# Optimization experiments

Measured on AMD Instinct MI355X. Metric: run time of the kernel, lower is better.

## Reference

```python
import jax, jax.numpy as jnp
import numpy as np

CD_W = 0.2  # chamfer_weight
EPS = 1e-7


def setup_inputs() -> dict:
    key = jax.random.key(0)
    k1, k2, k3, k4, k5 = jax.random.split(key, 5)
    B, N, K = 16, 4096, 4096
    num_add, obj_num_p = 8, 512
    return {
        "adv_pc": jax.random.normal(k1, (B, N, 3), dtype=jnp.float32),
        "ori_pc": jax.random.normal(k2, (B, K, 3), dtype=jnp.float32),
        "adv_obj": jax.random.normal(k3, (B, num_add, obj_num_p, 3), dtype=jnp.float32),
        "ori_obj": jax.random.normal(k4, (B, num_add, obj_num_p, 3), dtype=jnp.float32),
        "weights": jax.random.uniform(k5, (B,), dtype=jnp.float32),
    }


def reference(adv_pc, ori_pc, adv_obj, ori_obj, weights):
    B = adv_pc.shape[0]
    # --- Chamfer (method='adv2ori'): mean over adv points of min squared dist to ori ---
    a2 = jnp.sum(adv_pc * adv_pc, axis=-1)            # [B, N]
    o2 = jnp.sum(ori_pc * ori_pc, axis=-1)            # [B, K]
    cross = jnp.einsum('bnd,bkd->bnk', adv_pc, ori_pc)  # [B, N, K]
    sqdist = a2[:, :, None] + o2[:, None, :] - 2.0 * cross  # [B, N, K]
    loss1 = jnp.mean(jnp.min(sqdist, axis=2), axis=1)  # [B] adv->ori NN sq dist
    chamfer_loss = jnp.mean(loss1 * weights)
    # --- Global L2 dist between flattened adv/ori objects ---
    diff = adv_obj.reshape(B, -1, 3) - ori_obj.reshape(B, -1, 3)
    l2 = jnp.sqrt(jnp.sum(diff * diff, axis=(1, 2)) + EPS)  # [B]
    l2_loss = jnp.mean(l2 * weights)
    return l2_loss + CD_W * chamfer_loss
```

## Files before the change

kernel.cpp:

```cpp
#include <hip/hip_runtime.h>
#include <math.h>

typedef short bf16x8 __attribute__((ext_vector_type(8)));
typedef float f32x16 __attribute__((ext_vector_type(16)));
typedef unsigned int u32x4 __attribute__((ext_vector_type(4)));

#define B 16
#define N 4096
#define K 4096
#define OBJ_ELEMS (8*512*3)
#define OBJ_VEC4  (OBJ_ELEMS/4)
#define NSEG 32
#define NCHUNK (N/NSEG)
#define BLK 512
#define OBJ_V4_PER_BLK (OBJ_VEC4/NSEG)
#define CD_W 0.2f
#define EPS_F 1e-7f

#define CS_OFF 0
#define LS_OFF (B*NSEG)

__device__ __forceinline__ unsigned int cvt_pk_bf16(float lo, float hi) {
    unsigned int r;
    asm volatile("v_cvt_pk_bf16_f32 %0, %1, %2" : "=v"(r) : "v"(lo), "v"(hi));
    return r;
}

__global__ __launch_bounds__(BLK, 4) void chamfer_mfma_kernel(
    const float* __restrict__ adv, const float* __restrict__ ori,
    const float* __restrict__ adv_obj, const float* __restrict__ ori_obj,
    float* __restrict__ csum, float* __restrict__ lsq)
{
    __shared__ uint2 slds[K];
    __shared__ float rowmin[8][32];
    __shared__ float a2lds[NCHUNK];
    __shared__ float red_c[2], red_l[2];

    const int nseg = blockIdx.x;
    const int b    = blockIdx.y;
    const int tid  = threadIdx.x;
    const int wid  = tid >> 6;
    const int lane = tid & 63;
    const int col  = lane & 31;
    const int hi   = lane >> 5;
    const int rg   = wid & 3;
    const int kh   = wid >> 2;

    {
        const float4* src =
            reinterpret_cast<const float4*>(ori + (size_t)(b*K + tid*8)*3);
        float4 f0 = src[0], f1 = src[1], f2 = src[2];
        float4 f3 = src[3], f4 = src[4], f5 = src[5];
        float xs[8], ys[8], zs[8];
        xs[0]=f0.x; ys[0]=f0.y; zs[0]=f0.z;
        xs[1]=f0.w; ys[1]=f1.x; zs[1]=f1.y;
        xs[2]=f1.z; ys[2]=f1.w; zs[2]=f2.x;
        xs[3]=f2.y; ys[3]=f2.z; zs[3]=f2.w;
        xs[4]=f3.x; ys[4]=f3.y; zs[4]=f3.z;
        xs[5]=f3.w; ys[5]=f4.x; zs[5]=f4.y;
        xs[6]=f4.z; ys[6]=f4.w; zs[6]=f5.x;
        xs[7]=f5.y; ys[7]=f5.z; zs[7]=f5.w;
        #pragma unroll
        for (int j = 0; j < 8; ++j) {
            float x = xs[j], y = ys[j], z = zs[j];
            float o2 = x*x + y*y + z*z;
            uint2 e;
            e.x = cvt_pk_bf16(-2.f*x, -2.f*y);
            e.y = cvt_pk_bf16(-2.f*z, o2);
            slds[tid*8 + j] = e;
        }
    }

    const int n = nseg*NCHUNK + rg*32 + col;
    const float* ap = adv + (b*N + n)*3;
    float ax = ap[0], ay = ap[1], az = ap[2];
    float a2 = ax*ax + ay*ay + az*az;
    if (kh == 0 && hi == 0) a2lds[rg*32 + col] = a2;
    unsigned int a01 = 0u, a23 = 0u;
    if (hi == 0) {
        a01 = cvt_pk_bf16(ax, ay);
        a23 = cvt_pk_bf16(az, 1.0f);
    }
    u32x4 aw = {a01, a23, 0u, 0u};
    bf16x8 afrag = __builtin_bit_cast(bf16x8, aw);

    __syncthreads();

    f32x16 acc = {INFINITY,INFINITY,INFINITY,INFINITY,
                  INFINITY,INFINITY,INFINITY,INFINITY,
                  INFINITY,INFINITY,INFINITY,INFINITY,
                  INFINITY,INFINITY,INFINITY,INFINITY};
    const f32x16 zc = {0,0,0,0, 0,0,0,0, 0,0,0,0, 0,0,0,0};
    const float4* s4 = reinterpret_cast<const float4*>(slds);

    #pragma unroll
    for (int ph = 0; ph < 4; ++ph) {
        float4 f[8];
        #pragma unroll
        for (int j = 0; j < 8; ++j)
            f[j] = s4[(kh*32 + ph*8 + j)*32 + col];
        #pragma unroll
        for (int j = 0; j < 8; ++j) {
            u32x4 uu = __builtin_bit_cast(u32x4, f[j]);
            u32x4 w0 = {uu.x, uu.y, 0u, 0u};
            u32x4 w1 = {uu.z, uu.w, 0u, 0u};
            bf16x8 b0 = __builtin_bit_cast(bf16x8, w0);
            bf16x8 b1 = __builtin_bit_cast(bf16x8, w1);
            f32x16 c0 = __builtin_amdgcn_mfma_f32_32x32x16_bf16(afrag, b0, zc, 0,0,0);
            f32x16 c1 = __builtin_amdgcn_mfma_f32_32x32x16_bf16(afrag, b1, zc, 0,0,0);
            #pragma unroll
            for (int r = 0; r < 16; ++r)
                acc[r] = fminf(fminf(c0[r], c1[r]), acc[r]);
        }
    }

    #pragma unroll
    for (int r = 0; r < 16; ++r) {
        float v = acc[r];
        v = fminf(v, __shfl_xor(v, 1));
        v = fminf(v, __shfl_xor(v, 2));
        v = fminf(v, __shfl_xor(v, 4));
        v = fminf(v, __shfl_xor(v, 8));
        v = fminf(v, __shfl_xor(v, 16));
        acc[r] = v;
    }
    if (col == 0) {
        #pragma unroll
        for (int r = 0; r < 16; ++r)
            rowmin[wid][(r&3) + 8*(r>>2) + 4*hi] = acc[r];
    }
    __syncthreads();

    float s = 0.f;
    if (wid < 2) {
        int row = tid;
        int rg2 = row >> 5, ri = row & 31;
        float m = fminf(rowmin[rg2][ri], rowmin[4 + rg2][ri]);
        s = m + a2lds[row];
    } else if (wid < 4) {
        int li = (wid - 2)*64 + lane;
        if (li < OBJ_V4_PER_BLK) {
            int idx = b*OBJ_VEC4 + nseg*OBJ_V4_PER_BLK + li;
            float4 a = reinterpret_cast<const float4*>(adv_obj)[idx];
            float4 o = reinterpret_cast<const float4*>(ori_obj)[idx];
            float dx = a.x - o.x, dy = a.y - o.y, dz = a.z - o.z, dw = a.w - o.w;
            s = dx*dx + dy*dy + dz*dz + dw*dw;
        }
    }
    #pragma unroll
    for (int off = 32; off; off >>= 1) s += __shfl_down(s, off);
    if (lane == 0) {
        if (wid < 2)       red_c[wid]     = s;
        else if (wid < 4)  red_l[wid - 2] = s;
    }
    __syncthreads();
    if (tid == 0) csum[b*NSEG + nseg] = red_c[0] + red_c[1];
    if (tid == 1) lsq [b*NSEG + nseg] = red_l[0] + red_l[1];
}

__global__ __launch_bounds__(256) void final_kernel(
    const float* __restrict__ csum, const float* __restrict__ lsq,
    const float* __restrict__ w, float* __restrict__ out)
{
    const int tid = threadIdx.x;
    float c = csum[2*tid] + csum[2*tid + 1];
    float l = lsq [2*tid] + lsq [2*tid + 1];
    #pragma unroll
    for (int off = 8; off; off >>= 1) {
        c += __shfl_down(c, off, 16);
        l += __shfl_down(l, off, 16);
    }
    __shared__ float sc[B], sl[B];
    int bb = tid >> 4;
    if ((tid & 15) == 0) { sc[bb] = c; sl[bb] = l; }
    __syncthreads();
    if (tid < 64) {
        float cc = 0.f, ll = 0.f;
        if (tid < B) {
            float wt = w[tid];
            cc = (sc[tid] / (float)N) * wt;
            ll = sqrtf(sl[tid] + EPS_F) * wt;
        }
        #pragma unroll
        for (int off = 8; off; off >>= 1) {
            cc += __shfl_down(cc, off);
            ll += __shfl_down(ll, off);
        }
        if (tid == 0) out[0] = ll / (float)B + CD_W * (cc / (float)B);
    }
}

extern "C" void kernel_launch(void* const* d_in, const int* in_sizes, int n_in,
                              void* d_out, int out_size, void* d_ws, size_t ws_size,
                              hipStream_t stream)
{
    const float* adv_pc  = (const float*)d_in[0];
    const float* ori_pc  = (const float*)d_in[1];
    const float* adv_obj = (const float*)d_in[2];
    const float* ori_obj = (const float*)d_in[3];
    const float* weights = (const float*)d_in[4];
    float* out = (float*)d_out;
    float* ws  = (float*)d_ws;

    float* csum = ws + CS_OFF;
    float* lsq  = ws + LS_OFF;

    chamfer_mfma_kernel<<<dim3(NSEG, B), dim3(BLK), 0, stream>>>(
        adv_pc, ori_pc, adv_obj, ori_obj, csum, lsq);

    final_kernel<<<dim3(1), dim3(256), 0, stream>>>(csum, lsq, weights, out);
}
```

Measured before the change: 19.59 us.

## Fuse final reduction into main kernel via atomicAdd, compute L2 in nseg-0 blocks

Drops the separate final reduction kernel. Each block now scales its chamfer partial sum by the weight and constants and atomically adds it to the output, which is zeroed by a memset. The per-batch L2 object norm is computed entirely by the nseg==0 block (six waves, eight float4 loads each) so the sqrt can be applied locally. This trades one kernel launch for a memset, 512 float atomics, and a load imbalance in the nseg==0 blocks.

```diff
diff --git a/kernel.cpp b/kernel.cpp
--- a/kernel.cpp
+++ b/kernel.cpp
@@ -13,12 +13,8 @@
 #define NSEG 32
 #define NCHUNK (N/NSEG)
 #define BLK 512
-#define OBJ_V4_PER_BLK (OBJ_VEC4/NSEG)
 #define CD_W 0.2f
 #define EPS_F 1e-7f
-
-#define CS_OFF 0
-#define LS_OFF (B*NSEG)
 
 __device__ __forceinline__ unsigned int cvt_pk_bf16(float lo, float hi) {
     unsigned int r;
@@ -29,12 +25,12 @@
 __global__ __launch_bounds__(BLK, 4) void chamfer_mfma_kernel(
     const float* __restrict__ adv, const float* __restrict__ ori,
     const float* __restrict__ adv_obj, const float* __restrict__ ori_obj,
-    float* __restrict__ csum, float* __restrict__ lsq)
+    const float* __restrict__ w, float* __restrict__ out)
 {
     __shared__ uint2 slds[K];
     __shared__ float rowmin[8][32];
     __shared__ float a2lds[NCHUNK];
-    __shared__ float red_c[2], red_l[2];
+    __shared__ float red_c[2], red_l[6];
 
     const int nseg = blockIdx.x;
     const int b    = blockIdx.y;
@@ -137,56 +133,34 @@
         int rg2 = row >> 5, ri = row & 31;
         float m = fminf(rowmin[rg2][ri], rowmin[4 + rg2][ri]);
         s = m + a2lds[row];
-    } else if (wid < 4) {
-        int li = (wid - 2)*64 + lane;
-        if (li < OBJ_V4_PER_BLK) {
-            int idx = b*OBJ_VEC4 + nseg*OBJ_V4_PER_BLK + li;
+    } else if (nseg == 0) {
+        int i = (wid - 2)*64 + lane;
+        #pragma unroll
+        for (int j = 0; j < 8; ++j) {
+            int idx = b*OBJ_VEC4 + i + j*384;
             float4 a = reinterpret_cast<const float4*>(adv_obj)[idx];
             float4 o = reinterpret_cast<const float4*>(ori_obj)[idx];
             float dx = a.x - o.x, dy = a.y - o.y, dz = a.z - o.z, dw = a.w - o.w;
-            s = dx*dx + dy*dy + dz*dz + dw*dw;
+            s += dx*dx + dy*dy + dz*dz + dw*dw;
         }
     }
     #pragma unroll
     for (int off = 32; off; off >>= 1) s += __shfl_down(s, off);
     if (lane == 0) {
-        if (wid < 2)       red_c[wid]     = s;
-        else if (wid < 4)  red_l[wid - 2] = s;
+        if (wid < 2) red_c[wid]     = s;
+        else         red_l[wid - 2] = s;
     }
     __syncthreads();
-    if (tid == 0) csum[b*NSEG + nseg] = red_c[0] + red_c[1];
-    if (tid == 1) lsq [b*NSEG + nseg] = red_l[0] + red_l[1];
-}
 
-__global__ __launch_bounds__(256) void final_kernel(
-    const float* __restrict__ csum, const float* __restrict__ lsq,
-    const float* __restrict__ w, float* __restrict__ out)
-{
-    const int tid = threadIdx.x;
-    float c = csum[2*tid] + csum[2*tid + 1];
-    float l = lsq [2*tid] + lsq [2*tid + 1];
-    #pragma unroll
-    for (int off = 8; off; off >>= 1) {
-        c += __shfl_down(c, off, 16);
-        l += __shfl_down(l, off, 16);
-    }
-    __shared__ float sc[B], sl[B];
-    int bb = tid >> 4;
-    if ((tid & 15) == 0) { sc[bb] = c; sl[bb] = l; }
-    __syncthreads();
-    if (tid < 64) {
-        float cc = 0.f, ll = 0.f;
-        if (tid < B) {
-            float wt = w[tid];
-            cc = (sc[tid] / (float)N) * wt;
-            ll = sqrtf(sl[tid] + EPS_F) * wt;
+    if (tid == 0) {
+        float wt = w[b];
+        float contrib = (red_c[0] + red_c[1]) * wt * (CD_W / ((float)B * (float)N));
+        if (nseg == 0) {
+            float lsum = red_l[0] + red_l[1] + red_l[2]
+                       + red_l[3] + red_l[4] + red_l[5];
+            contrib += sqrtf(lsum + EPS_F) * wt / (float)B;
         }
-        #pragma unroll
-        for (int off = 8; off; off >>= 1) {
-            cc += __shfl_down(cc, off);
-            ll += __shfl_down(ll, off);
-        }
-        if (tid == 0) out[0] = ll / (float)B + CD_W * (cc / (float)B);
+        atomicAdd(out, contrib);
     }
 }
 
@@ -200,13 +174,9 @@
     const float* ori_obj = (const float*)d_in[3];
     const float* weights = (const float*)d_in[4];
     float* out = (float*)d_out;
-    float* ws  = (float*)d_ws;
 
-    float* csum = ws + CS_OFF;
-    float* lsq  = ws + LS_OFF;
+    hipMemsetAsync(out, 0, sizeof(float), stream);
 
     chamfer_mfma_kernel<<<dim3(NSEG, B), dim3(BLK), 0, stream>>>(
-        adv_pc, ori_pc, adv_obj, ori_obj, csum, lsq);
-
-    final_kernel<<<dim3(1), dim3(256), 0, stream>>>(csum, lsq, weights, out);
+        adv_pc, ori_pc, adv_obj, ori_obj, weights, out);
 }
```

Result: slower. 24.46 us (+24.8%).

## Prepack ori points to bf16 in separate kernel, read from global instead of LDS

Applied to the files above, without the earlier changes.

Adds a pre-pass kernel that converts ori points into packed bf16 (-2x,-2y,-2z,|o|^2) once per batch and writes them to workspace. The main kernel drops its per-block LDS staging and barrier and instead loads the packed operands directly from global memory (likely L2-resident). This removes the 32x redundant conversion per batch and the LDS footprint, at the cost of an extra kernel launch and global/L2 loads in the inner loop instead of LDS reads.

```diff
diff --git a/kernel.cpp b/kernel.cpp
--- a/kernel.cpp
+++ b/kernel.cpp
@@ -19,6 +19,7 @@
 
 #define CS_OFF 0
 #define LS_OFF (B*NSEG)
+#define PK_OFF 2048
 
 __device__ __forceinline__ unsigned int cvt_pk_bf16(float lo, float hi) {
     unsigned int r;
@@ -26,12 +27,24 @@
     return r;
 }
 
+__global__ __launch_bounds__(256) void pack_ori_kernel(
+    const float* __restrict__ ori, uint2* __restrict__ packed)
+{
+    int i = blockIdx.x * 256 + threadIdx.x;
+    const float* s = ori + (size_t)i*3;
+    float x = s[0], y = s[1], z = s[2];
+    float o2 = x*x + y*y + z*z;
+    uint2 e;
+    e.x = cvt_pk_bf16(-2.f*x, -2.f*y);
+    e.y = cvt_pk_bf16(-2.f*z, o2);
+    packed[i] = e;
+}
+
 __global__ __launch_bounds__(BLK, 4) void chamfer_mfma_kernel(
-    const float* __restrict__ adv, const float* __restrict__ ori,
+    const float* __restrict__ adv, const uint2* __restrict__ packed,
     const float* __restrict__ adv_obj, const float* __restrict__ ori_obj,
     float* __restrict__ csum, float* __restrict__ lsq)
 {
-    __shared__ uint2 slds[K];
     __shared__ float rowmin[8][32];
     __shared__ float a2lds[NCHUNK];
     __shared__ float red_c[2], red_l[2];
@@ -46,33 +59,8 @@
     const int rg   = wid & 3;
     const int kh   = wid >> 2;
 
-    {
-        const float4* src =
-            reinterpret_cast<const float4*>(ori + (size_t)(b*K + tid*8)*3);
-        float4 f0 = src[0], f1 = src[1], f2 = src[2];
-        float4 f3 = src[3], f4 = src[4], f5 = src[5];
-        float xs[8], ys[8], zs[8];
-        xs[0]=f0.x; ys[0]=f0.y; zs[0]=f0.z;
-        xs[1]=f0.w; ys[1]=f1.x; zs[1]=f1.y;
-        xs[2]=f1.z; ys[2]=f1.w; zs[2]=f2.x;
-        xs[3]=f2.y; ys[3]=f2.z; zs[3]=f2.w;
-        xs[4]=f3.x; ys[4]=f3.y; zs[4]=f3.z;
-        xs[5]=f3.w; ys[5]=f4.x; zs[5]=f4.y;
-        xs[6]=f4.z; ys[6]=f4.w; zs[6]=f5.x;
-        xs[7]=f5.y; ys[7]=f5.z; zs[7]=f5.w;
-        #pragma unroll
-        for (int j = 0; j < 8; ++j) {
-            float x = xs[j], y = ys[j], z = zs[j];
-            float o2 = x*x + y*y + z*z;
-            uint2 e;
-            e.x = cvt_pk_bf16(-2.f*x, -2.f*y);
-            e.y = cvt_pk_bf16(-2.f*z, o2);
-            slds[tid*8 + j] = e;
-        }
-    }
-
     const int n = nseg*NCHUNK + rg*32 + col;
-    const float* ap = adv + (b*N + n)*3;
+    const float* ap = adv + (size_t)(b*N + n)*3;
     float ax = ap[0], ay = ap[1], az = ap[2];
     float a2 = ax*ax + ay*ay + az*az;
     if (kh == 0 && hi == 0) a2lds[rg*32 + col] = a2;
@@ -84,24 +72,22 @@
     u32x4 aw = {a01, a23, 0u, 0u};
     bf16x8 afrag = __builtin_bit_cast(bf16x8, aw);
 
-    __syncthreads();
-
     f32x16 acc = {INFINITY,INFINITY,INFINITY,INFINITY,
                   INFINITY,INFINITY,INFINITY,INFINITY,
                   INFINITY,INFINITY,INFINITY,INFINITY,
                   INFINITY,INFINITY,INFINITY,INFINITY};
     const f32x16 zc = {0,0,0,0, 0,0,0,0, 0,0,0,0, 0,0,0,0};
-    const float4* s4 = reinterpret_cast<const float4*>(slds);
+    const u32x4* gb4 = reinterpret_cast<const u32x4*>(packed + (size_t)b*K);
 
     #pragma unroll
     for (int ph = 0; ph < 4; ++ph) {
-        float4 f[8];
+        u32x4 f[8];
         #pragma unroll
         for (int j = 0; j < 8; ++j)
-            f[j] = s4[(kh*32 + ph*8 + j)*32 + col];
+            f[j] = gb4[(kh*32 + ph*8 + j)*32 + col];
         #pragma unroll
         for (int j = 0; j < 8; ++j) {
-            u32x4 uu = __builtin_bit_cast(u32x4, f[j]);
+            u32x4 uu = f[j];
             u32x4 w0 = {uu.x, uu.y, 0u, 0u};
             u32x4 w1 = {uu.z, uu.w, 0u, 0u};
             bf16x8 b0 = __builtin_bit_cast(bf16x8, w0);
@@ -202,11 +188,14 @@
     float* out = (float*)d_out;
     float* ws  = (float*)d_ws;
 
-    float* csum = ws + CS_OFF;
-    float* lsq  = ws + LS_OFF;
+    float* csum   = ws + CS_OFF;
+    float* lsq    = ws + LS_OFF;
+    uint2* packed = (uint2*)(ws + PK_OFF);
+
+    pack_ori_kernel<<<dim3(B*K/256), dim3(256), 0, stream>>>(ori_pc, packed);
 
     chamfer_mfma_kernel<<<dim3(NSEG, B), dim3(BLK), 0, stream>>>(
-        adv_pc, ori_pc, adv_obj, ori_obj, csum, lsq);
+        adv_pc, packed, adv_obj, ori_obj, csum, lsq);
 
     final_kernel<<<dim3(1), dim3(256), 0, stream>>>(csum, lsq, weights, out);
 }
```

Result: slower. 23.38 us (+19.3%).

## Swap MFMA operands so per-row min reduces in-lane without cross-lane shuffles

Applied to the files above, without the earlier changes.

Swaps the A/B operands of the bf16 MFMA so the ori points become the row dimension and each adv point occupies an output column. The min over ori points can then be taken almost entirely within each lane's accumulator registers using a min3 tree, followed by a single xor-32 shuffle. This replaces the 16x5 cross-lane shuffle reduction and the a2 shared-memory staging. The cost is a larger per-iteration min3 tree in the inner loop.

```diff
diff --git a/kernel.cpp b/kernel.cpp
--- a/kernel.cpp
+++ b/kernel.cpp
@@ -20,6 +20,8 @@
 #define CS_OFF 0
 #define LS_OFF (B*NSEG)
 
+#define MIN3(a,b,c) fminf(fminf((a),(b)),(c))
+
 __device__ __forceinline__ unsigned int cvt_pk_bf16(float lo, float hi) {
     unsigned int r;
     asm volatile("v_cvt_pk_bf16_f32 %0, %1, %2" : "=v"(r) : "v"(lo), "v"(hi));
@@ -33,7 +35,6 @@
 {
     __shared__ uint2 slds[K];
     __shared__ float rowmin[8][32];
-    __shared__ float a2lds[NCHUNK];
     __shared__ float red_c[2], red_l[2];
 
     const int nseg = blockIdx.x;
@@ -72,24 +73,20 @@
     }
 
     const int n = nseg*NCHUNK + rg*32 + col;
-    const float* ap = adv + (b*N + n)*3;
+    const float* ap = adv + (size_t)(b*N + n)*3;
     float ax = ap[0], ay = ap[1], az = ap[2];
     float a2 = ax*ax + ay*ay + az*az;
-    if (kh == 0 && hi == 0) a2lds[rg*32 + col] = a2;
     unsigned int a01 = 0u, a23 = 0u;
     if (hi == 0) {
         a01 = cvt_pk_bf16(ax, ay);
         a23 = cvt_pk_bf16(az, 1.0f);
     }
     u32x4 aw = {a01, a23, 0u, 0u};
-    bf16x8 afrag = __builtin_bit_cast(bf16x8, aw);
-
-    __syncthreads();
-
-    f32x16 acc = {INFINITY,INFINITY,INFINITY,INFINITY,
-                  INFINITY,INFINITY,INFINITY,INFINITY,
-                  INFINITY,INFINITY,INFINITY,INFINITY,
-                  INFINITY,INFINITY,INFINITY,INFINITY};
+    bf16x8 bfrag = __builtin_bit_cast(bf16x8, aw);
+
+    __syncthreads();
+
+    float m = INFINITY;
     const f32x16 zc = {0,0,0,0, 0,0,0,0, 0,0,0,0, 0,0,0,0};
     const float4* s4 = reinterpret_cast<const float4*>(slds);
 
@@ -104,39 +101,40 @@
             u32x4 uu = __builtin_bit_cast(u32x4, f[j]);
             u32x4 w0 = {uu.x, uu.y, 0u, 0u};
             u32x4 w1 = {uu.z, uu.w, 0u, 0u};
-            bf16x8 b0 = __builtin_bit_cast(bf16x8, w0);
-            bf16x8 b1 = __builtin_bit_cast(bf16x8, w1);
-            f32x16 c0 = __builtin_amdgcn_mfma_f32_32x32x16_bf16(afrag, b0, zc, 0,0,0);
-            f32x16 c1 = __builtin_amdgcn_mfma_f32_32x32x16_bf16(afrag, b1, zc, 0,0,0);
-            #pragma unroll
-            for (int r = 0; r < 16; ++r)
-                acc[r] = fminf(fminf(c0[r], c1[r]), acc[r]);
-        }
-    }
-
-    #pragma unroll
-    for (int r = 0; r < 16; ++r) {
-        float v = acc[r];
-        v = fminf(v, __shfl_xor(v, 1));
-        v = fminf(v, __shfl_xor(v, 2));
-        v = fminf(v, __shfl_xor(v, 4));
-        v = fminf(v, __shfl_xor(v, 8));
-        v = fminf(v, __shfl_xor(v, 16));
-        acc[r] = v;
-    }
-    if (col == 0) {
-        #pragma unroll
-        for (int r = 0; r < 16; ++r)
-            rowmin[wid][(r&3) + 8*(r>>2) + 4*hi] = acc[r];
-    }
+            bf16x8 t0 = __builtin_bit_cast(bf16x8, w0);
+            bf16x8 t1 = __builtin_bit_cast(bf16x8, w1);
+            f32x16 c0 = __builtin_amdgcn_mfma_f32_32x32x16_bf16(t0, bfrag, zc, 0,0,0);
+            f32x16 c1 = __builtin_amdgcn_mfma_f32_32x32x16_bf16(t1, bfrag, zc, 0,0,0);
+            #define V(i) ((i) < 16 ? c0[(i)] : c1[(i)-16])
+            float g0 = MIN3(V(0),  V(1),  V(2));
+            float g1 = MIN3(V(3),  V(4),  V(5));
+            float g2 = MIN3(V(6),  V(7),  V(8));
+            float g3 = MIN3(V(9),  V(10), V(11));
+            float g4 = MIN3(V(12), V(13), V(14));
+            float g5 = MIN3(V(15), V(16), V(17));
+            float g6 = MIN3(V(18), V(19), V(20));
+            float g7 = MIN3(V(21), V(22), V(23));
+            float g8 = MIN3(V(24), V(25), V(26));
+            float g9 = MIN3(V(27), V(28), V(29));
+            float h0 = MIN3(g0, g1, g2);
+            float h1 = MIN3(g3, g4, g5);
+            float h2 = MIN3(g6, g7, g8);
+            float h3 = MIN3(g9, V(30), V(31));
+            m = MIN3(MIN3(h0, h1, h2), h3, m);
+            #undef V
+        }
+    }
+
+    m = fminf(m, __shfl_xor(m, 32));
+    m += a2;
+    if (hi == 0) rowmin[wid][col] = m;
     __syncthreads();
 
     float s = 0.f;
     if (wid < 2) {
         int row = tid;
         int rg2 = row >> 5, ri = row & 31;
-        float m = fminf(rowmin[rg2][ri], rowmin[4 + rg2][ri]);
-        s = m + a2lds[row];
+        s = fminf(rowmin[rg2][ri], rowmin[4 + rg2][ri]);
     } else if (wid < 4) {
         int li = (wid - 2)*64 + lane;
         if (li < OBJ_V4_PER_BLK) {
```

New measurement: 16.71 us. 1.17x faster.
